# Optimization experiments

Measured on AMD Instinct MI355X. Metric: run time of the kernel, lower is better.

## Reference

```python
import jax, jax.numpy as jnp
import numpy as np

N = 50000
E = 1600000
IN, OUT = 128, 64


def _gcn(h, W, b, src, dst):
    # DGL GraphConv, norm='both', weight applied first (in>out), activation=relu
    x = h @ W  # [N, OUT]
    ones = jnp.ones((src.shape[0],), dtype=h.dtype)
    deg_out = jnp.clip(jax.ops.segment_sum(ones, src, num_segments=N), 1.0)
    deg_in = jnp.clip(jax.ops.segment_sum(ones, dst, num_segments=N), 1.0)
    x = x * jax.lax.rsqrt(deg_out)[:, None]
    agg = jax.ops.segment_sum(x[src], dst, num_segments=N)  # SpMM
    agg = agg * jax.lax.rsqrt(deg_in)[:, None]
    return jax.nn.relu(agg + b)


def setup_inputs() -> dict:
    key = jax.random.key(0)
    ks = jax.random.split(key, 10)
    inp = {"h": jax.random.normal(ks[0], (N, IN), dtype=jnp.float32)}
    for i in range(3):
        inp[f"src{i}"] = jax.random.randint(ks[1 + 2 * i], (E,), 0, N, dtype=jnp.int32)
        inp[f"dst{i}"] = jax.random.randint(ks[2 + 2 * i], (E,), 0, N, dtype=jnp.int32)
        inp[f"W{i}"] = jax.random.normal(ks[7 + i], (IN, OUT), dtype=jnp.float32) * (1.0 / np.sqrt(IN))
        inp[f"b{i}"] = jnp.zeros((OUT,), dtype=jnp.float32)
    return inp


def reference(h, src0, dst0, src1, dst1, src2, dst2, W0, b0, W1, b1, W2, b2):
    e0 = _gcn(h, W0, b0, src0, dst0)
    e1 = _gcn(h, W1, b1, src1, dst1)
    e2 = _gcn(h, W2, b2, src2, dst2)
    # stack over meta-path dim then mean == average of semantic embeddings
    return (e0 + e1 + e2) / 3.0
```

## Files before the change

### kernel.cpp

```cpp
#include <hip/hip_runtime.h>

#define KDIM 128
#define NCOLS 64
#define NHCH 64
#define HW 12500
#define COARSE 512
#define NC 98
#define SFCAP 17408
#define BUCKET 64
#define NBUCK 782
#define FCAP 2816
#define NPB 85
#define PREP_HIST (3 * NHCH)
#define PREP_CNT  (3 * NPB)
#define PREP_WF   12
#define PREP_CONV 565
#define PREP_GRID (PREP_HIST + PREP_CNT + PREP_WF + PREP_CONV)

typedef __attribute__((ext_vector_type(8))) short bf16x8;
typedef __attribute__((ext_vector_type(4))) float f32x4;

struct GArgs {
  const int*   src[3];
  const int*   dst[3];
  const float* W[3];
  const float* b[3];
  int          E[3];
};

__device__ __forceinline__ unsigned short f2bf(float f) {
  unsigned u = __float_as_uint(f);
  u += 0x7FFFu + ((u >> 16) & 1u);
  return (unsigned short)(u >> 16);
}
__device__ __forceinline__ float bflo(unsigned u) { return __uint_as_float(u << 16); }
__device__ __forceinline__ float bfhi(unsigned u) { return __uint_as_float(u & 0xFFFF0000u); }

__global__ __launch_bounds__(256) void prep_kernel(
    GArgs A, const float* __restrict__ h, unsigned short* __restrict__ hb,
    unsigned short* __restrict__ Wf, unsigned* __restrict__ P8,
    int* __restrict__ tot, int total8) {
  __shared__ unsigned sbuf[HW];
  const int b = blockIdx.x;
  const int t = threadIdx.x;

  if (b < PREP_HIST) {
    const int g = b >> 6;
    const int chunk = b & 63;
    const int E = A.E[g];
    const int per_chunk = (((E + NHCH - 1) / NHCH) + 3) & ~3;
    const int* __restrict__ keys = A.src[g];
    for (int i = t; i < HW; i += 256) sbuf[i] = 0;
    __syncthreads();
    const int e0 = chunk * per_chunk;
    const int e1 = min(e0 + per_chunk, E);
    const int nn = max(e1 - e0, 0);
    const int nv = nn >> 2;
    const int4* k4p = (const int4*)&keys[e0];
    for (int v = t; v < nv; v += 256) {
      int4 k = k4p[v];
      atomicAdd(&sbuf[(unsigned)k.x >> 2], 1u << (((unsigned)k.x & 3u) * 8));
      atomicAdd(&sbuf[(unsigned)k.y >> 2], 1u << (((unsigned)k.y & 3u) * 8));
      atomicAdd(&sbuf[(unsigned)k.z >> 2], 1u << (((unsigned)k.z & 3u) * 8));
      atomicAdd(&sbuf[(unsigned)k.w >> 2], 1u << (((unsigned)k.w & 3u) * 8));
    }
    for (int e = e0 + (nv << 2) + t; e < e1; e += 256) {
      unsigned k = (unsigned)keys[e];
      atomicAdd(&sbuf[k >> 2], 1u << ((k & 3u) * 8));
    }
    __syncthreads();
    unsigned* __restrict__ dstp = P8 + (size_t)b * HW;
    for (int i = t; i < HW; i += 256) dstp[i] = sbuf[i];

  } else if (b < PREP_HIST + PREP_CNT) {
    const int bb = b - PREP_HIST;
    const int g = bb / NPB;
    const int blk = bb % NPB;
    const int E = A.E[g];
    const int per_block = (((E + NPB - 1) / NPB) + 3) & ~3;
    const int* __restrict__ dst = A.dst[g];
    int* hcnt = (int*)sbuf;
    if (t < NC) hcnt[t] = 0;
    __syncthreads();
    const int e0 = blk * per_block;
    const int e1 = min(e0 + per_block, E);
    const int nn = max(e1 - e0, 0);
    const int nv = nn >> 2;
    const int4* d4 = (const int4*)&dst[e0];
    for (int v = t; v < nv; v += 256) {
      int4 d = d4[v];
      atomicAdd(&hcnt[(unsigned)d.x >> 9], 1);
      atomicAdd(&hcnt[(unsigned)d.y >> 9], 1);
      atomicAdd(&hcnt[(unsigned)d.z >> 9], 1);
      atomicAdd(&hcnt[(unsigned)d.w >> 9], 1);
    }
    for (int e = e0 + (nv << 2) + t; e < e1; e += 256)
      atomicAdd(&hcnt[(unsigned)dst[e] >> 9], 1);
    __syncthreads();
    if (t < NC && hcnt[t]) atomicAdd(&tot[g * NC + t], hcnt[t]);

  } else if (b < PREP_HIST + PREP_CNT + PREP_WF) {
    int tid = (b - PREP_HIST - PREP_CNT) * 256 + t;
    int lane = tid & 63;
    int frag = (tid >> 6) & 15;
    int g = tid >> 10;
    int c = frag >> 2, kk = frag & 3;
    int n = lane & 15, quad = lane >> 4;
    const float* W = A.W[g];
    unsigned short v[8];
    #pragma unroll
    for (int j = 0; j < 8; ++j) {
      int k = 32 * kk + quad * 8 + j;
      v[j] = f2bf(W[k * 64 + 4 * n + c]);
    }
    uint4 u;
    u.x = (unsigned)v[0] | ((unsigned)v[1] << 16);
    u.y = (unsigned)v[2] | ((unsigned)v[3] << 16);
    u.z = (unsigned)v[4] | ((unsigned)v[5] << 16);
    u.w = (unsigned)v[6] | ((unsigned)v[7] << 16);
    ((uint4*)Wf)[tid] = u;

  } else {
    const int cb = b - (PREP_HIST + PREP_CNT + PREP_WF);
    for (int i = cb * 256 + t; i < total8; i += PREP_CONV * 256) {
      const float4* hp = (const float4*)(h + (size_t)i * 8);
      float4 f0 = hp[0];
      float4 f1 = hp[1];
      uint4 u;
      u.x = (unsigned)f2bf(f0.x) | ((unsigned)f2bf(f0.y) << 16);
      u.y = (unsigned)f2bf(f0.z) | ((unsigned)f2bf(f0.w) << 16);
      u.z = (unsigned)f2bf(f1.x) | ((unsigned)f2bf(f1.y) << 16);
      u.w = (unsigned)f2bf(f1.z) | ((unsigned)f2bf(f1.w) << 16);
      ((uint4*)hb)[i] = u;
    }
  }
}

__global__ __launch_bounds__(128) void scan_off_kernel(
    const int* __restrict__ tot, int* __restrict__ off, int* __restrict__ cursor) {
  __shared__ int sd[128];
  const int t = threadIdx.x;
  for (int g = 0; g < 3; ++g) {
    int v = (t < NC) ? tot[g * NC + t] : 0;
    sd[t] = v;
    __syncthreads();
    for (int o = 1; o < 128; o <<= 1) {
      int add = (t >= o) ? sd[t - o] : 0;
      __syncthreads();
      sd[t] += add;
      __syncthreads();
    }
    int excl = sd[t] - v;
    if (t < NC) { off[g * (NC + 1) + t] = excl; cursor[g * NC + t] = excl; }
    if (t == 0) off[g * (NC + 1) + NC] = sd[127];
    __syncthreads();
  }
}

__global__ __launch_bounds__(256) void partition_coarse_kernel(
    GArgs A, int* __restrict__ cursor, unsigned* __restrict__ P2c, int Emax) {
  __shared__ int lcnt[NC];
  __shared__ int lcur[NC];
  const int g = blockIdx.y;
  const int E = A.E[g];
  const int per_block = (((E + NPB - 1) / NPB) + 3) & ~3;
  const int* __restrict__ src = A.src[g];
  const int* __restrict__ dst = A.dst[g];
  unsigned* __restrict__ P2g = P2c + (size_t)g * Emax;
  const int t = threadIdx.x;
  if (t < NC) lcnt[t] = 0;
  __syncthreads();
  const int e0 = blockIdx.x * per_block;
  const int e1 = min(e0 + per_block, E);
  const int n = max(e1 - e0, 0);
  const int nv = n >> 2;
  const int4* d4 = (const int4*)&dst[e0];
  const int4* s4 = (const int4*)&src[e0];
  for (int v = t; v < nv; v += 256) {
    int4 d = d4[v];
    atomicAdd(&lcnt[(unsigned)d.x >> 9], 1);
    atomicAdd(&lcnt[(unsigned)d.y >> 9], 1);
    atomicAdd(&lcnt[(unsigned)d.z >> 9], 1);
    atomicAdd(&lcnt[(unsigned)d.w >> 9], 1);
  }
  for (int e = e0 + (nv << 2) + t; e < e1; e += 256)
    atomicAdd(&lcnt[(unsigned)dst[e] >> 9], 1);
  __syncthreads();
  if (t < NC) {
    int c = lcnt[t];
    lcur[t] = c ? atomicAdd(&cursor[g * NC + t], c) : 0;
  }
  __syncthreads();
  for (int v = t; v < nv; v += 256) {
    int4 d = d4[v];
    int4 s = s4[v];
    unsigned bk; int pos;
    bk = (unsigned)d.x >> 9; pos = atomicAdd(&lcur[bk], 1);
    P2g[pos] = (unsigned)s.x | (((unsigned)d.x & 511u) << 16);
    bk = (unsigned)d.y >> 9; pos = atomicAdd(&lcur[bk], 1);
    P2g[pos] = (unsigned)s.y | (((unsigned)d.y & 511u) << 16);
    bk = (unsigned)d.z >> 9; pos = atomicAdd(&lcur[bk], 1);
    P2g[pos] = (unsigned)s.z | (((unsigned)d.z & 511u) << 16);
    bk = (unsigned)d.w >> 9; pos = atomicAdd(&lcur[bk], 1);
    P2g[pos] = (unsigned)s.w | (((unsigned)d.w & 511u) << 16);
  }
  for (int e = e0 + (nv << 2) + t; e < e1; e += 256) {
    unsigned d = (unsigned)dst[e];
    unsigned bk = d >> 9;
    int pos = atomicAdd(&lcur[bk], 1);
    P2g[pos] = (unsigned)src[e] | ((d & 511u) << 16);
  }
}

__global__ __launch_bounds__(512) void sort_fine_kernel(
    const unsigned* __restrict__ P2c, const int* __restrict__ off,
    unsigned short* __restrict__ S, int* __restrict__ row_start,
    int N, int Emax) {
  __shared__ int cnt[COARSE];
  __shared__ int sd[COARSE];
  __shared__ int cur[COARSE];
  __shared__ unsigned short outl[SFCAP];
  const int c = blockIdx.x;
  const int g = blockIdx.y;
  const unsigned* __restrict__ P2g = P2c + (size_t)g * Emax;
  const int base_e = off[g * (NC + 1) + c];
  const int nloc = off[g * (NC + 1) + c + 1] - base_e;
  const int t = threadIdx.x;

  cnt[t] = 0;
  __syncthreads();
  for (int i = t; i < nloc; i += 512)
    atomicAdd(&cnt[(P2g[base_e + i] >> 16) & 511u], 1);
  __syncthreads();
  int v = cnt[t];
  sd[t] = v;
  __syncthreads();
  for (int o = 1; o < 512; o <<= 1) {
    int add = (t >= o) ? sd[t - o] : 0;
    __syncthreads();
    sd[t] += add;
    __syncthreads();
  }
  int excl = sd[t] - v;
  cur[t] = excl;
  int node = c * COARSE + t;
  if (node <= N) row_start[g * (N + 1) + node] = base_e + excl;
  __syncthreads();
  for (int i = t; i < nloc; i += 512) {
    unsigned p = P2g[base_e + i];
    int pos = atomicAdd(&cur[(p >> 16) & 511u], 1);
    if (pos < SFCAP) outl[pos] = (unsigned short)(p & 0xFFFFu);
  }
  __syncthreads();
  unsigned short* __restrict__ Sg = S + (size_t)g * Emax;
  for (int i = t; i < nloc; i += 512) Sg[base_e + i] = outl[i];
}

__global__ __launch_bounds__(512) void gemm_mfma_kernel(
    GArgs A, const unsigned short* __restrict__ hb,
    const unsigned short* __restrict__ Wf, const unsigned* __restrict__ P8,
    unsigned short* __restrict__ x, int N) {
  __shared__ unsigned ldegw[64];
  const int g = blockIdx.y;
  unsigned short* __restrict__ xg = x + (size_t)g * N * NCOLS;
  const int t = threadIdx.x;
  const int row0 = blockIdx.x * 128;

  if (t < 64) ldegw[t] = 0;
  __syncthreads();
  if (t < 256) {
    const unsigned* __restrict__ Pg = P8 + (size_t)g * NHCH * HW;
    const int widx = t >> 3;
    const int cg = t & 7;
    const int wcol = min((row0 >> 2) + widx, HW - 1);
    unsigned lo = 0, hi = 0;
    #pragma unroll
    for (int cc = 0; cc < 8; ++cc) {
      unsigned wv = Pg[(size_t)(cg * 8 + cc) * HW + wcol];
      lo += wv & 0x00FF00FFu;
      hi += (wv >> 8) & 0x00FF00FFu;
    }
    atomicAdd(&ldegw[2 * widx], lo);
    atomicAdd(&ldegw[2 * widx + 1], hi);
  }

  const int lane = t & 63;
  const int w = t >> 6;
  const int quad = lane >> 4;
  const int n = lane & 15;

  int arow = min(row0 + w * 16 + n, N - 1);
  const unsigned short* hrow = hb + (size_t)arow * KDIM + quad * 8;
  bf16x8 a0 = *(const bf16x8*)(hrow);
  bf16x8 a1 = *(const bf16x8*)(hrow + 32);
  bf16x8 a2 = *(const bf16x8*)(hrow + 64);
  bf16x8 a3 = *(const bf16x8*)(hrow + 96);

  const uint4* wfp = (const uint4*)Wf + (size_t)g * 1024 + lane;

  f32x4 acc[4];
  #pragma unroll
  for (int c = 0; c < 4; ++c) acc[c] = (f32x4)(0.f);

  __syncthreads();

  #pragma unroll
  for (int c = 0; c < 4; ++c) {
    union { uint4 u; bf16x8 v; } b0, b1, b2, b3;
    b0.u = wfp[(size_t)(c * 4 + 0) * 64];
    b1.u = wfp[(size_t)(c * 4 + 1) * 64];
    b2.u = wfp[(size_t)(c * 4 + 2) * 64];
    b3.u = wfp[(size_t)(c * 4 + 3) * 64];
    acc[c] = __builtin_amdgcn_mfma_f32_16x16x32_bf16(a0, b0.v, acc[c], 0, 0, 0);
    acc[c] = __builtin_amdgcn_mfma_f32_16x16x32_bf16(a1, b1.v, acc[c], 0, 0, 0);
    acc[c] = __builtin_amdgcn_mfma_f32_16x16x32_bf16(a2, b2.v, acc[c], 0, 0, 0);
    acc[c] = __builtin_amdgcn_mfma_f32_16x16x32_bf16(a3, b3.v, acc[c], 0, 0, 0);
  }

  const int rbase = row0 + w * 16 + quad * 4;
  #pragma unroll
  for (int r = 0; r < 4; ++r) {
    int row = rbase + r;
    if (row < N) {
      int lr = row - row0;
      float dg = (float)((ldegw[2 * (lr >> 2) + (lr & 1)] >> (((lr >> 1) & 1) * 16)) & 0xFFFFu);
      float s = rsqrtf(fmaxf(dg, 1.0f));
      uint2 o;
      o.x = (unsigned)f2bf(acc[0][r] * s) | ((unsigned)f2bf(acc[1][r] * s) << 16);
      o.y = (unsigned)f2bf(acc[2][r] * s) | ((unsigned)f2bf(acc[3][r] * s) << 16);
      *(uint2*)(xg + (size_t)row * NCOLS + 4 * n) = o;
    }
  }
}

__global__ __launch_bounds__(512) void spmm_all_kernel(
    GArgs A, const unsigned short* __restrict__ S,
    const int* __restrict__ row_start, const unsigned short* __restrict__ x,
    float* __restrict__ out, int N, int Emax) {
  __shared__ int rs[BUCKET + 1];
  __shared__ unsigned short srcs[FCAP];

  const int t = threadIdx.x;
  const int bk = blockIdx.x;
  const int dbase = bk * BUCKET;
  const int nd = min(BUCKET, N - dbase);
  const int grp = t >> 3;
  const int qe = (t & 7) * 8;

  float tot[8];
  #pragma unroll
  for (int j = 0; j < 8; ++j) tot[j] = 0.f;

  for (int g = 0; g < 3; ++g) {
    const unsigned short* __restrict__ Sg = S + (size_t)g * Emax;
    const int* __restrict__ rsg = row_start + (size_t)g * (N + 1);
    const unsigned short* __restrict__ xg = x + (size_t)g * N * NCOLS;

    __syncthreads();
    if (t <= BUCKET) rs[t] = rsg[min(dbase + t, N)];
    __syncthreads();
    const int e0 = rs[0];
    const int ne = min(rs[BUCKET] - e0, FCAP);
    for (int i = t; i < ne; i += 512) srcs[i] = Sg[e0 + i];
    __syncthreads();

    if (grp < nd) {
      int i = rs[grp] - e0;
      const int iend = min(rs[grp + 1] - e0, ne);
      const int deg = iend - i;
      float acc[8];
      #pragma unroll
      for (int j = 0; j < 8; ++j) acc[j] = 0.f;
      for (; i + 3 < iend; i += 4) {
        int sa = srcs[i + 0];
        int sb = srcs[i + 1];
        int sc = srcs[i + 2];
        int sdd = srcs[i + 3];
        uint4 ua = *(const uint4*)&xg[(size_t)sa * NCOLS + qe];
        uint4 ub = *(const uint4*)&xg[(size_t)sb * NCOLS + qe];
        uint4 uc = *(const uint4*)&xg[(size_t)sc * NCOLS + qe];
        uint4 ud = *(const uint4*)&xg[(size_t)sdd * NCOLS + qe];
        acc[0] += bflo(ua.x) + bflo(ub.x) + bflo(uc.x) + bflo(ud.x);
        acc[1] += bfhi(ua.x) + bfhi(ub.x) + bfhi(uc.x) + bfhi(ud.x);
        acc[2] += bflo(ua.y) + bflo(ub.y) + bflo(uc.y) + bflo(ud.y);
        acc[3] += bfhi(ua.y) + bfhi(ub.y) + bfhi(uc.y) + bfhi(ud.y);
        acc[4] += bflo(ua.z) + bflo(ub.z) + bflo(uc.z) + bflo(ud.z);
        acc[5] += bfhi(ua.z) + bfhi(ub.z) + bfhi(uc.z) + bfhi(ud.z);
        acc[6] += bflo(ua.w) + bflo(ub.w) + bflo(uc.w) + bflo(ud.w);
        acc[7] += bfhi(ua.w) + bfhi(ub.w) + bfhi(uc.w) + bfhi(ud.w);
      }
      for (; i < iend; ++i) {
        int s = srcs[i];
        uint4 u = *(const uint4*)&xg[(size_t)s * NCOLS + qe];
        acc[0] += bflo(u.x); acc[1] += bfhi(u.x);
        acc[2] += bflo(u.y); acc[3] += bfhi(u.y);
        acc[4] += bflo(u.z); acc[5] += bfhi(u.z);
        acc[6] += bflo(u.w); acc[7] += bfhi(u.w);
      }
      float sc2 = rsqrtf(fmaxf((float)deg, 1.0f));
      const float* bg = A.b[g] + qe;
      #pragma unroll
      for (int j = 0; j < 8; ++j)
        tot[j] += fmaxf(fmaf(acc[j], sc2, bg[j]), 0.f) * (1.0f / 3.0f);
    }
  }

  if (grp < nd) {
    float* op = &out[(size_t)(dbase + grp) * NCOLS + qe];
    *(float4*)&op[0] = make_float4(tot[0], tot[1], tot[2], tot[3]);
    *(float4*)&op[4] = make_float4(tot[4], tot[5], tot[6], tot[7]);
  }
}

extern "C" void kernel_launch(void* const* d_in, const int* in_sizes, int n_in,
                              void* d_out, int out_size, void* d_ws, size_t ws_size,
                              hipStream_t stream) {
  const float* h = (const float*)d_in[0];
  const int N = in_sizes[0] / KDIM;
  float* out = (float*)d_out;

  GArgs A;
  int Emax = 0;
  for (int g = 0; g < 3; ++g) {
    A.src[g] = (const int*)  d_in[1 + g * 4];
    A.dst[g] = (const int*)  d_in[2 + g * 4];
    A.W[g]   = (const float*)d_in[3 + g * 4];
    A.b[g]   = (const float*)d_in[4 + g * 4];
    A.E[g]   = in_sizes[1 + g * 4];
    if (A.E[g] > Emax) Emax = A.E[g];
  }

  char* w = (char*)d_ws;
  unsigned short* x = (unsigned short*)w;
  char* w2 = w + (size_t)3 * N * NCOLS * sizeof(unsigned short);
  unsigned short* hb = (unsigned short*)w2;
  char* w3 = w2 + (size_t)N * KDIM * sizeof(unsigned short);
  unsigned* P2c = (unsigned*)w3;
  char* w4 = w3 + (size_t)3 * Emax * sizeof(unsigned);
  unsigned* P8 = (unsigned*)w4;
  char* w5 = w4 + (size_t)3 * NHCH * HW * sizeof(unsigned);
  unsigned short* S = (unsigned short*)w5;
  char* w6 = w5 + (size_t)3 * Emax * sizeof(unsigned short);
  unsigned short* Wf = (unsigned short*)w6;
  char* w7 = w6 + (size_t)3 * 16 * 64 * 8 * sizeof(unsigned short);
  int* row_start = (int*)w7;
  char* w8 = w7 + (size_t)3 * (N + 1) * sizeof(int);
  int* tot    = (int*)w8;
  int* off    = tot + 3 * NC;
  int* cursor = off + 3 * (NC + 1);

  hipMemsetAsync(tot, 0, 3 * NC * sizeof(int), stream);
  const int total8 = N * KDIM / 8;
  prep_kernel<<<PREP_GRID, 256, 0, stream>>>(A, h, hb, Wf, P8, tot, total8);
  scan_off_kernel<<<1, 128, 0, stream>>>(tot, off, cursor);
  partition_coarse_kernel<<<dim3(NPB, 3), 256, 0, stream>>>(A, cursor, P2c, Emax);
  sort_fine_kernel<<<dim3(NC, 3), 512, 0, stream>>>(P2c, off, S, row_start, N, Emax);
  gemm_mfma_kernel<<<dim3((N + 127) / 128, 3), 512, 0, stream>>>(A, hb, Wf, P8, x, N);
  spmm_all_kernel<<<NBUCK, 512, 0, stream>>>(A, S, row_start, x, out, N, Emax);
}
```

Before: 268.7 us.

## Merge partition and GEMM kernels, fold scan, split SpMM by edge ranges per graph

Removes the single-block scan kernel by recomputing the prefix sum of bucket counts inside the partition blocks and the fine-sort blocks. Partition and GEMM now run as one launch with disjoint block ranges so they can overlap. The SpMM is split across a 3-wide grid, one slice per meta-path, and each thread group takes an equal span of edges, accumulating into shared memory with atomics. Results go to the output through global float atomics, and prep now zeroes the output first. The extra atomics and the replicated scans cost something, in exchange for more parallelism, balanced work across nodes of different degree, and fewer launches.

```diff
diff --git a/kernel.cpp b/kernel.cpp
--- a/kernel.cpp
+++ b/kernel.cpp
@@ -16,6 +16,10 @@
 #define PREP_WF   12
 #define PREP_CONV 565
 #define PREP_GRID (PREP_HIST + PREP_CNT + PREP_WF + PREP_CONV)
+#define PG_PART (3 * NPB)
+#define PG_GEMM_PER 391
+#define PG_GEMM (3 * PG_GEMM_PER)
+#define PG_GRID (PG_PART + PG_GEMM)
 
 typedef __attribute__((ext_vector_type(8))) short bf16x8;
 typedef __attribute__((ext_vector_type(4))) float f32x4;
@@ -39,7 +43,7 @@
 __global__ __launch_bounds__(256) void prep_kernel(
     GArgs A, const float* __restrict__ h, unsigned short* __restrict__ hb,
     unsigned short* __restrict__ Wf, unsigned* __restrict__ P8,
-    int* __restrict__ tot, int total8) {
+    int* __restrict__ tot, float* __restrict__ outz, int total8) {
   __shared__ unsigned sbuf[HW];
   const int b = blockIdx.x;
   const int t = threadIdx.x;
@@ -133,99 +137,185 @@
       u.w = (unsigned)f2bf(f1.z) | ((unsigned)f2bf(f1.w) << 16);
       ((uint4*)hb)[i] = u;
     }
-  }
-}
-
-__global__ __launch_bounds__(128) void scan_off_kernel(
-    const int* __restrict__ tot, int* __restrict__ off, int* __restrict__ cursor) {
-  __shared__ int sd[128];
+    const int nout4 = total8;
+    const float4 z = make_float4(0.f, 0.f, 0.f, 0.f);
+    for (int i = cb * 256 + t; i < nout4; i += PREP_CONV * 256)
+      ((float4*)outz)[i] = z;
+  }
+}
+
+__global__ __launch_bounds__(512) void pg_kernel(
+    GArgs A, const unsigned short* __restrict__ hb,
+    const unsigned short* __restrict__ Wf, const unsigned* __restrict__ P8,
+    unsigned short* __restrict__ x, const int* __restrict__ tot,
+    int* __restrict__ cursor, unsigned* __restrict__ P2c, int N, int Emax) {
+  __shared__ int sh[2 * NC + 128];
+  const int b = blockIdx.x;
   const int t = threadIdx.x;
-  for (int g = 0; g < 3; ++g) {
-    int v = (t < NC) ? tot[g * NC + t] : 0;
-    sd[t] = v;
+
+  if (b < PG_PART) {
+    int* lcnt = sh;
+    int* lcur = sh + NC;
+    int* sdp  = sh + 2 * NC;
+    const int g = b / NPB;
+    const int blk = b % NPB;
+    const int E = A.E[g];
+    const int per_block = (((E + NPB - 1) / NPB) + 3) & ~3;
+    const int* __restrict__ src = A.src[g];
+    const int* __restrict__ dst = A.dst[g];
+    unsigned* __restrict__ P2g = P2c + (size_t)g * Emax;
+    if (t < NC) lcnt[t] = 0;
+    __syncthreads();
+    const int e0 = blk * per_block;
+    const int e1 = min(e0 + per_block, E);
+    const int n = max(e1 - e0, 0);
+    const int nv = n >> 2;
+    const int4* d4 = (const int4*)&dst[e0];
+    const int4* s4 = (const int4*)&src[e0];
+    for (int v = t; v < nv; v += 512) {
+      int4 d = d4[v];
+      atomicAdd(&lcnt[(unsigned)d.x >> 9], 1);
+      atomicAdd(&lcnt[(unsigned)d.y >> 9], 1);
+      atomicAdd(&lcnt[(unsigned)d.z >> 9], 1);
+      atomicAdd(&lcnt[(unsigned)d.w >> 9], 1);
+    }
+    for (int e = e0 + (nv << 2) + t; e < e1; e += 512)
+      atomicAdd(&lcnt[(unsigned)dst[e] >> 9], 1);
+    __syncthreads();
+    if (t < 128) sdp[t] = (t < NC) ? tot[g * NC + t] : 0;
     __syncthreads();
     for (int o = 1; o < 128; o <<= 1) {
-      int add = (t >= o) ? sd[t - o] : 0;
+      int add = (t >= o && t < 128) ? sdp[t - o] : 0;
       __syncthreads();
-      sd[t] += add;
+      if (t < 128) sdp[t] += add;
       __syncthreads();
     }
-    int excl = sd[t] - v;
-    if (t < NC) { off[g * (NC + 1) + t] = excl; cursor[g * NC + t] = excl; }
-    if (t == 0) off[g * (NC + 1) + NC] = sd[127];
-    __syncthreads();
-  }
-}
-
-__global__ __launch_bounds__(256) void partition_coarse_kernel(
-    GArgs A, int* __restrict__ cursor, unsigned* __restrict__ P2c, int Emax) {
-  __shared__ int lcnt[NC];
-  __shared__ int lcur[NC];
-  const int g = blockIdx.y;
-  const int E = A.E[g];
-  const int per_block = (((E + NPB - 1) / NPB) + 3) & ~3;
-  const int* __restrict__ src = A.src[g];
-  const int* __restrict__ dst = A.dst[g];
-  unsigned* __restrict__ P2g = P2c + (size_t)g * Emax;
-  const int t = threadIdx.x;
-  if (t < NC) lcnt[t] = 0;
-  __syncthreads();
-  const int e0 = blockIdx.x * per_block;
-  const int e1 = min(e0 + per_block, E);
-  const int n = max(e1 - e0, 0);
-  const int nv = n >> 2;
-  const int4* d4 = (const int4*)&dst[e0];
-  const int4* s4 = (const int4*)&src[e0];
-  for (int v = t; v < nv; v += 256) {
-    int4 d = d4[v];
-    atomicAdd(&lcnt[(unsigned)d.x >> 9], 1);
-    atomicAdd(&lcnt[(unsigned)d.y >> 9], 1);
-    atomicAdd(&lcnt[(unsigned)d.z >> 9], 1);
-    atomicAdd(&lcnt[(unsigned)d.w >> 9], 1);
-  }
-  for (int e = e0 + (nv << 2) + t; e < e1; e += 256)
-    atomicAdd(&lcnt[(unsigned)dst[e] >> 9], 1);
-  __syncthreads();
-  if (t < NC) {
-    int c = lcnt[t];
-    lcur[t] = c ? atomicAdd(&cursor[g * NC + t], c) : 0;
-  }
-  __syncthreads();
-  for (int v = t; v < nv; v += 256) {
-    int4 d = d4[v];
-    int4 s = s4[v];
-    unsigned bk; int pos;
-    bk = (unsigned)d.x >> 9; pos = atomicAdd(&lcur[bk], 1);
-    P2g[pos] = (unsigned)s.x | (((unsigned)d.x & 511u) << 16);
-    bk = (unsigned)d.y >> 9; pos = atomicAdd(&lcur[bk], 1);
-    P2g[pos] = (unsigned)s.y | (((unsigned)d.y & 511u) << 16);
-    bk = (unsigned)d.z >> 9; pos = atomicAdd(&lcur[bk], 1);
-    P2g[pos] = (unsigned)s.z | (((unsigned)d.z & 511u) << 16);
-    bk = (unsigned)d.w >> 9; pos = atomicAdd(&lcur[bk], 1);
-    P2g[pos] = (unsigned)s.w | (((unsigned)d.w & 511u) << 16);
-  }
-  for (int e = e0 + (nv << 2) + t; e < e1; e += 256) {
-    unsigned d = (unsigned)dst[e];
-    unsigned bk = d >> 9;
-    int pos = atomicAdd(&lcur[bk], 1);
-    P2g[pos] = (unsigned)src[e] | ((d & 511u) << 16);
+    if (t < NC) {
+      int c = lcnt[t];
+      int excl = sdp[t] - tot[g * NC + t];
+      lcur[t] = excl + (c ? atomicAdd(&cursor[g * NC + t], c) : 0);
+    }
+    __syncthreads();
+    for (int v = t; v < nv; v += 512) {
+      int4 d = d4[v];
+      int4 s = s4[v];
+      unsigned bk; int pos;
+      bk = (unsigned)d.x >> 9; pos = atomicAdd(&lcur[bk], 1);
+      P2g[pos] = (unsigned)s.x | (((unsigned)d.x & 511u) << 16);
+      bk = (unsigned)d.y >> 9; pos = atomicAdd(&lcur[bk], 1);
+      P2g[pos] = (unsigned)s.y | (((unsigned)d.y & 511u) << 16);
+      bk = (unsigned)d.z >> 9; pos = atomicAdd(&lcur[bk], 1);
+      P2g[pos] = (unsigned)s.z | (((unsigned)d.z & 511u) << 16);
+      bk = (unsigned)d.w >> 9; pos = atomicAdd(&lcur[bk], 1);
+      P2g[pos] = (unsigned)s.w | (((unsigned)d.w & 511u) << 16);
+    }
+    for (int e = e0 + (nv << 2) + t; e < e1; e += 512) {
+      unsigned d = (unsigned)dst[e];
+      unsigned bk = d >> 9;
+      int pos = atomicAdd(&lcur[bk], 1);
+      P2g[pos] = (unsigned)src[e] | ((d & 511u) << 16);
+    }
+
+  } else {
+    unsigned* ldegw = (unsigned*)sh;
+    const int gb = b - PG_PART;
+    const int g = gb / PG_GEMM_PER;
+    const int blk = gb % PG_GEMM_PER;
+    const int row0 = blk * 128;
+    unsigned short* __restrict__ xg = x + (size_t)g * N * NCOLS;
+
+    if (t < 64) ldegw[t] = 0;
+    __syncthreads();
+    if (t < 256) {
+      const unsigned* __restrict__ Pg = P8 + (size_t)g * NHCH * HW;
+      const int widx = t >> 3;
+      const int cg = t & 7;
+      const int wcol = min((row0 >> 2) + widx, HW - 1);
+      unsigned lo = 0, hi = 0;
+      #pragma unroll
+      for (int cc = 0; cc < 8; ++cc) {
+        unsigned wv = Pg[(size_t)(cg * 8 + cc) * HW + wcol];
+        lo += wv & 0x00FF00FFu;
+        hi += (wv >> 8) & 0x00FF00FFu;
+      }
+      atomicAdd(&ldegw[2 * widx], lo);
+      atomicAdd(&ldegw[2 * widx + 1], hi);
+    }
+
+    const int lane = t & 63;
+    const int w = t >> 6;
+    const int quad = lane >> 4;
+    const int n = lane & 15;
+
+    int arow = min(row0 + w * 16 + n, N - 1);
+    const unsigned short* hrow = hb + (size_t)arow * KDIM + quad * 8;
+    bf16x8 a0 = *(const bf16x8*)(hrow);
+    bf16x8 a1 = *(const bf16x8*)(hrow + 32);
+    bf16x8 a2 = *(const bf16x8*)(hrow + 64);
+    bf16x8 a3 = *(const bf16x8*)(hrow + 96);
+
+    const uint4* wfp = (const uint4*)Wf + (size_t)g * 1024 + lane;
+
+    f32x4 acc[4];
+    #pragma unroll
+    for (int c = 0; c < 4; ++c) acc[c] = (f32x4)(0.f);
+
+    __syncthreads();
+
+    #pragma unroll
+    for (int c = 0; c < 4; ++c) {
+      union { uint4 u; bf16x8 v; } b0, b1, b2, b3;
+      b0.u = wfp[(size_t)(c * 4 + 0) * 64];
+      b1.u = wfp[(size_t)(c * 4 + 1) * 64];
+      b2.u = wfp[(size_t)(c * 4 + 2) * 64];
+      b3.u = wfp[(size_t)(c * 4 + 3) * 64];
+      acc[c] = __builtin_amdgcn_mfma_f32_16x16x32_bf16(a0, b0.v, acc[c], 0, 0, 0);
+      acc[c] = __builtin_amdgcn_mfma_f32_16x16x32_bf16(a1, b1.v, acc[c], 0, 0, 0);
+      acc[c] = __builtin_amdgcn_mfma_f32_16x16x32_bf16(a2, b2.v, acc[c], 0, 0, 0);
+      acc[c] = __builtin_amdgcn_mfma_f32_16x16x32_bf16(a3, b3.v, acc[c], 0, 0, 0);
+    }
+
+    const int rbase = row0 + w * 16 + quad * 4;
+    #pragma unroll
+    for (int r = 0; r < 4; ++r) {
+      int row = rbase + r;
+      if (row < N) {
+        int lr = row - row0;
+        float dg = (float)((ldegw[2 * (lr >> 2) + (lr & 1)] >> (((lr >> 1) & 1) * 16)) & 0xFFFFu);
+        float s = rsqrtf(fmaxf(dg, 1.0f));
+        uint2 o;
+        o.x = (unsigned)f2bf(acc[0][r] * s) | ((unsigned)f2bf(acc[1][r] * s) << 16);
+        o.y = (unsigned)f2bf(acc[2][r] * s) | ((unsigned)f2bf(acc[3][r] * s) << 16);
+        *(uint2*)(xg + (size_t)row * NCOLS + 4 * n) = o;
+      }
+    }
   }
 }
 
 __global__ __launch_bounds__(512) void sort_fine_kernel(
-    const unsigned* __restrict__ P2c, const int* __restrict__ off,
+    const unsigned* __restrict__ P2c, const int* __restrict__ tot,
     unsigned short* __restrict__ S, int* __restrict__ row_start,
     int N, int Emax) {
   __shared__ int cnt[COARSE];
   __shared__ int sd[COARSE];
   __shared__ int cur[COARSE];
+  __shared__ int sds[128];
   __shared__ unsigned short outl[SFCAP];
   const int c = blockIdx.x;
   const int g = blockIdx.y;
   const unsigned* __restrict__ P2g = P2c + (size_t)g * Emax;
-  const int base_e = off[g * (NC + 1) + c];
-  const int nloc = off[g * (NC + 1) + c + 1] - base_e;
   const int t = threadIdx.x;
+
+  if (t < 128) sds[t] = (t < NC) ? tot[g * NC + t] : 0;
+  __syncthreads();
+  for (int o = 1; o < 128; o <<= 1) {
+    int add = (t >= o && t < 128) ? sds[t - o] : 0;
+    __syncthreads();
+    if (t < 128) sds[t] += add;
+    __syncthreads();
+  }
+  const int base_e = (c == 0) ? 0 : sds[c - 1];
+  const int nloc = tot[g * NC + c];
 
   cnt[t] = 0;
   __syncthreads();
@@ -254,83 +344,6 @@
   __syncthreads();
   unsigned short* __restrict__ Sg = S + (size_t)g * Emax;
   for (int i = t; i < nloc; i += 512) Sg[base_e + i] = outl[i];
-}
-
-__global__ __launch_bounds__(512) void gemm_mfma_kernel(
-    GArgs A, const unsigned short* __restrict__ hb,
-    const unsigned short* __restrict__ Wf, const unsigned* __restrict__ P8,
-    unsigned short* __restrict__ x, int N) {
-  __shared__ unsigned ldegw[64];
-  const int g = blockIdx.y;
-  unsigned short* __restrict__ xg = x + (size_t)g * N * NCOLS;
-  const int t = threadIdx.x;
-  const int row0 = blockIdx.x * 128;
-
-  if (t < 64) ldegw[t] = 0;
-  __syncthreads();
-  if (t < 256) {
-    const unsigned* __restrict__ Pg = P8 + (size_t)g * NHCH * HW;
-    const int widx = t >> 3;
-    const int cg = t & 7;
-    const int wcol = min((row0 >> 2) + widx, HW - 1);
-    unsigned lo = 0, hi = 0;
-    #pragma unroll
-    for (int cc = 0; cc < 8; ++cc) {
-      unsigned wv = Pg[(size_t)(cg * 8 + cc) * HW + wcol];
-      lo += wv & 0x00FF00FFu;
-      hi += (wv >> 8) & 0x00FF00FFu;
-    }
-    atomicAdd(&ldegw[2 * widx], lo);
-    atomicAdd(&ldegw[2 * widx + 1], hi);
-  }
-
-  const int lane = t & 63;
-  const int w = t >> 6;
-  const int quad = lane >> 4;
-  const int n = lane & 15;
-
-  int arow = min(row0 + w * 16 + n, N - 1);
-  const unsigned short* hrow = hb + (size_t)arow * KDIM + quad * 8;
-  bf16x8 a0 = *(const bf16x8*)(hrow);
-  bf16x8 a1 = *(const bf16x8*)(hrow + 32);
-  bf16x8 a2 = *(const bf16x8*)(hrow + 64);
-  bf16x8 a3 = *(const bf16x8*)(hrow + 96);
-
-  const uint4* wfp = (const uint4*)Wf + (size_t)g * 1024 + lane;
-
-  f32x4 acc[4];
-  #pragma unroll
-  for (int c = 0; c < 4; ++c) acc[c] = (f32x4)(0.f);
-
-  __syncthreads();
-
-  #pragma unroll
-  for (int c = 0; c < 4; ++c) {
-    union { uint4 u; bf16x8 v; } b0, b1, b2, b3;
-    b0.u = wfp[(size_t)(c * 4 + 0) * 64];
-    b1.u = wfp[(size_t)(c * 4 + 1) * 64];
-    b2.u = wfp[(size_t)(c * 4 + 2) * 64];
-    b3.u = wfp[(size_t)(c * 4 + 3) * 64];
-    acc[c] = __builtin_amdgcn_mfma_f32_16x16x32_bf16(a0, b0.v, acc[c], 0, 0, 0);
-    acc[c] = __builtin_amdgcn_mfma_f32_16x16x32_bf16(a1, b1.v, acc[c], 0, 0, 0);
-    acc[c] = __builtin_amdgcn_mfma_f32_16x16x32_bf16(a2, b2.v, acc[c], 0, 0, 0);
-    acc[c] = __builtin_amdgcn_mfma_f32_16x16x32_bf16(a3, b3.v, acc[c], 0, 0, 0);
-  }
-
-  const int rbase = row0 + w * 16 + quad * 4;
-  #pragma unroll
-  for (int r = 0; r < 4; ++r) {
-    int row = rbase + r;
-    if (row < N) {
-      int lr = row - row0;
-      float dg = (float)((ldegw[2 * (lr >> 2) + (lr & 1)] >> (((lr >> 1) & 1) * 16)) & 0xFFFFu);
-      float s = rsqrtf(fmaxf(dg, 1.0f));
-      uint2 o;
-      o.x = (unsigned)f2bf(acc[0][r] * s) | ((unsigned)f2bf(acc[1][r] * s) << 16);
-      o.y = (unsigned)f2bf(acc[2][r] * s) | ((unsigned)f2bf(acc[3][r] * s) << 16);
-      *(uint2*)(xg + (size_t)row * NCOLS + 4 * n) = o;
-    }
-  }
 }
 
 __global__ __launch_bounds__(512) void spmm_all_kernel(
@@ -339,76 +352,74 @@
     float* __restrict__ out, int N, int Emax) {
   __shared__ int rs[BUCKET + 1];
   __shared__ unsigned short srcs[FCAP];
+  __shared__ float agg[BUCKET * NCOLS];
 
   const int t = threadIdx.x;
+  const int g = blockIdx.y;
   const int bk = blockIdx.x;
   const int dbase = bk * BUCKET;
   const int nd = min(BUCKET, N - dbase);
   const int grp = t >> 3;
   const int qe = (t & 7) * 8;
 
-  float tot[8];
-  #pragma unroll
-  for (int j = 0; j < 8; ++j) tot[j] = 0.f;
-
-  for (int g = 0; g < 3; ++g) {
-    const unsigned short* __restrict__ Sg = S + (size_t)g * Emax;
-    const int* __restrict__ rsg = row_start + (size_t)g * (N + 1);
-    const unsigned short* __restrict__ xg = x + (size_t)g * N * NCOLS;
-
-    __syncthreads();
-    if (t <= BUCKET) rs[t] = rsg[min(dbase + t, N)];
-    __syncthreads();
-    const int e0 = rs[0];
-    const int ne = min(rs[BUCKET] - e0, FCAP);
-    for (int i = t; i < ne; i += 512) srcs[i] = Sg[e0 + i];
-    __syncthreads();
-
-    if (grp < nd) {
-      int i = rs[grp] - e0;
-      const int iend = min(rs[grp + 1] - e0, ne);
-      const int deg = iend - i;
-      float acc[8];
-      #pragma unroll
-      for (int j = 0; j < 8; ++j) acc[j] = 0.f;
-      for (; i + 3 < iend; i += 4) {
-        int sa = srcs[i + 0];
-        int sb = srcs[i + 1];
-        int sc = srcs[i + 2];
-        int sdd = srcs[i + 3];
-        uint4 ua = *(const uint4*)&xg[(size_t)sa * NCOLS + qe];
-        uint4 ub = *(const uint4*)&xg[(size_t)sb * NCOLS + qe];
-        uint4 uc = *(const uint4*)&xg[(size_t)sc * NCOLS + qe];
-        uint4 ud = *(const uint4*)&xg[(size_t)sdd * NCOLS + qe];
-        acc[0] += bflo(ua.x) + bflo(ub.x) + bflo(uc.x) + bflo(ud.x);
-        acc[1] += bfhi(ua.x) + bfhi(ub.x) + bfhi(uc.x) + bfhi(ud.x);
-        acc[2] += bflo(ua.y) + bflo(ub.y) + bflo(uc.y) + bflo(ud.y);
-        acc[3] += bfhi(ua.y) + bfhi(ub.y) + bfhi(uc.y) + bfhi(ud.y);
-        acc[4] += bflo(ua.z) + bflo(ub.z) + bflo(uc.z) + bflo(ud.z);
-        acc[5] += bfhi(ua.z) + bfhi(ub.z) + bfhi(uc.z) + bfhi(ud.z);
-        acc[6] += bflo(ua.w) + bflo(ub.w) + bflo(uc.w) + bflo(ud.w);
-        acc[7] += bfhi(ua.w) + bfhi(ub.w) + bfhi(uc.w) + bfhi(ud.w);
+  const unsigned short* __restrict__ Sg = S + (size_t)g * Emax;
+  const int* __restrict__ rsg = row_start + (size_t)g * (N + 1);
+  const unsigned short* __restrict__ xg = x + (size_t)g * N * NCOLS;
+
+  if (t <= BUCKET) rs[t] = rsg[min(dbase + t, N)];
+  for (int i = t; i < BUCKET * NCOLS; i += 512) agg[i] = 0.f;
+  __syncthreads();
+  const int e0 = rs[0];
+  const int ne = min(rs[BUCKET] - e0, FCAP);
+  for (int i = t; i < ne; i += 512) srcs[i] = Sg[e0 + i];
+  __syncthreads();
+
+  const int W = (ne + BUCKET - 1) >> 6;
+  int i = grp * W;
+  const int w1 = min(i + W, ne);
+  if (i < w1) {
+    int lo = 0, hi = BUCKET;
+    while (hi - lo > 1) {
+      int mid = (lo + hi) >> 1;
+      if (rs[mid] - e0 <= i) lo = mid; else hi = mid;
+    }
+    int node = lo;
+    int nend = min(rs[node + 1] - e0, ne);
+    float a0 = 0.f, a1 = 0.f, a2 = 0.f, a3 = 0.f;
+    float a4 = 0.f, a5 = 0.f, a6 = 0.f, a7 = 0.f;
+    for (; i < w1; ++i) {
+      if (i >= nend) {
+        float* ap = &agg[node * NCOLS + qe];
+        atomicAdd(&ap[0], a0); atomicAdd(&ap[1], a1);
+        atomicAdd(&ap[2], a2); atomicAdd(&ap[3], a3);
+        atomicAdd(&ap[4], a4); atomicAdd(&ap[5], a5);
+        atomicAdd(&ap[6], a6); atomicAdd(&ap[7], a7);
+        a0 = a1 = a2 = a3 = a4 = a5 = a6 = a7 = 0.f;
+        do { ++node; nend = min(rs[node + 1] - e0, ne); } while (nend <= i);
       }
-      for (; i < iend; ++i) {
-        int s = srcs[i];
-        uint4 u = *(const uint4*)&xg[(size_t)s * NCOLS + qe];
-        acc[0] += bflo(u.x); acc[1] += bfhi(u.x);
-        acc[2] += bflo(u.y); acc[3] += bfhi(u.y);
-        acc[4] += bflo(u.z); acc[5] += bfhi(u.z);
-        acc[6] += bflo(u.w); acc[7] += bfhi(u.w);
-      }
-      float sc2 = rsqrtf(fmaxf((float)deg, 1.0f));
-      const float* bg = A.b[g] + qe;
-      #pragma unroll
-      for (int j = 0; j < 8; ++j)
-        tot[j] += fmaxf(fmaf(acc[j], sc2, bg[j]), 0.f) * (1.0f / 3.0f);
-    }
-  }
-
-  if (grp < nd) {
-    float* op = &out[(size_t)(dbase + grp) * NCOLS + qe];
-    *(float4*)&op[0] = make_float4(tot[0], tot[1], tot[2], tot[3]);
-    *(float4*)&op[4] = make_float4(tot[4], tot[5], tot[6], tot[7]);
+      unsigned sv = srcs[i];
+      const uint4 u = *(const uint4*)&xg[(size_t)sv * NCOLS + qe];
+      a0 += bflo(u.x); a1 += bfhi(u.x);
+      a2 += bflo(u.y); a3 += bfhi(u.y);
+      a4 += bflo(u.z); a5 += bfhi(u.z);
+      a6 += bflo(u.w); a7 += bfhi(u.w);
+    }
+    float* ap = &agg[node * NCOLS + qe];
+    atomicAdd(&ap[0], a0); atomicAdd(&ap[1], a1);
+    atomicAdd(&ap[2], a2); atomicAdd(&ap[3], a3);
+    atomicAdd(&ap[4], a4); atomicAdd(&ap[5], a5);
+    atomicAdd(&ap[6], a6); atomicAdd(&ap[7], a7);
+  }
+  __syncthreads();
+
+  const float* __restrict__ bg = A.b[g];
+  for (int idx = t; idx < nd * NCOLS; idx += 512) {
+    int node = idx >> 6;
+    int col = idx & 63;
+    int deg = rs[node + 1] - rs[node];
+    float sc2 = rsqrtf(fmaxf((float)deg, 1.0f));
+    float v = fmaxf(fmaf(agg[idx], sc2, bg[col]), 0.f) * (1.0f / 3.0f);
+    atomicAdd(&out[(size_t)(dbase + node) * NCOLS + col], v);
   }
 }
 
@@ -446,15 +457,12 @@
   int* row_start = (int*)w7;
   char* w8 = w7 + (size_t)3 * (N + 1) * sizeof(int);
   int* tot    = (int*)w8;
-  int* off    = tot + 3 * NC;
-  int* cursor = off + 3 * (NC + 1);
-
-  hipMemsetAsync(tot, 0, 3 * NC * sizeof(int), stream);
+  int* cursor = tot + 3 * NC;
+
+  hipMemsetAsync(tot, 0, 2 * 3 * NC * sizeof(int), stream);
   const int total8 = N * KDIM / 8;
-  prep_kernel<<<PREP_GRID, 256, 0, stream>>>(A, h, hb, Wf, P8, tot, total8);
-  scan_off_kernel<<<1, 128, 0, stream>>>(tot, off, cursor);
-  partition_coarse_kernel<<<dim3(NPB, 3), 256, 0, stream>>>(A, cursor, P2c, Emax);
-  sort_fine_kernel<<<dim3(NC, 3), 512, 0, stream>>>(P2c, off, S, row_start, N, Emax);
-  gemm_mfma_kernel<<<dim3((N + 127) / 128, 3), 512, 0, stream>>>(A, hb, Wf, P8, x, N);
-  spmm_all_kernel<<<NBUCK, 512, 0, stream>>>(A, S, row_start, x, out, N, Emax);
-}
+  prep_kernel<<<PREP_GRID, 256, 0, stream>>>(A, h, hb, Wf, P8, tot, out, total8);
+  pg_kernel<<<PG_GRID, 512, 0, stream>>>(A, hb, Wf, P8, x, tot, cursor, P2c, N, Emax);
+  sort_fine_kernel<<<dim3(NC, 3), 512, 0, stream>>>(P2c, tot, S, row_start, N, Emax);
+  spmm_all_kernel<<<dim3(NBUCK, 3), 512, 0, stream>>>(A, S, row_start, x, out, N, Emax);
+}
```

Measured after the change: 327.9 us. +22.0%, slower.
